# Kernel optimization log

Measured on AMD Instinct MI355X. Metric: run time of the kernel, lower is better.

The kernel has to match this reference:

```python
import jax, jax.numpy as jnp
import numpy as np

N, E, H, IN, ED = 10000, 160000, 8, 128, 32
C1, C2 = 128, 128  # per-head channels of conv1 and conv2_1


def gat_conv(x, edge_index, edge_attr, W, We, att_s, att_d, att_e, bias, concat):
    """PyG GATConv with edge_dim, add_self_loops=True (fill_value='mean'), eval mode."""
    n = x.shape[0]
    h, c = att_s.shape
    src, dst = edge_index[0], edge_index[1]
    # self-loop edge_attr = per-node mean of incoming edge attrs (PyG fill_value='mean')
    deg = jax.ops.segment_sum(jnp.ones((src.shape[0],), x.dtype), dst, num_segments=n)
    loop_attr = jax.ops.segment_sum(edge_attr, dst, num_segments=n) / jnp.maximum(deg, 1.0)[:, None]
    loop = jnp.arange(n)
    src = jnp.concatenate([src, loop])
    dst = jnp.concatenate([dst, loop])
    ea = jnp.concatenate([edge_attr, loop_attr], axis=0)  # [E+N, ED]

    xh = (x @ W).reshape(n, h, c)                  # [N,H,C]
    a_s = jnp.sum(xh * att_s, axis=-1)             # [N,H]
    a_d = jnp.sum(xh * att_d, axis=-1)             # [N,H]
    eh = (ea @ We).reshape(-1, h, c)               # [E+N,H,C]
    a_e = jnp.sum(eh * att_e, axis=-1)             # [E+N,H]

    alpha = jax.nn.leaky_relu(a_s[src] + a_d[dst] + a_e, negative_slope=0.2)
    # segment softmax over incoming edges of each dst node (every node has a self loop)
    amax = jax.ops.segment_max(alpha, dst, num_segments=n)
    ex = jnp.exp(alpha - amax[dst])
    denom = jax.ops.segment_sum(ex, dst, num_segments=n)
    alpha = ex / (denom[dst] + 1e-16)

    out = jax.ops.segment_sum(xh[src] * alpha[:, :, None], dst, num_segments=n)  # [N,H,C]
    out = out.reshape(n, h * c) if concat else out.mean(axis=1)
    return out + bias


def setup_inputs() -> dict:
    key = jax.random.key(0)
    ks = jax.random.split(key, 16)
    s = 0.05
    return {
        "x": jax.random.normal(ks[0], (N, IN), jnp.float32),
        "edge_index": jax.random.randint(ks[1], (2, E), 0, N, dtype=jnp.int64),
        "edge_attr": jax.random.normal(ks[2], (E, ED), jnp.float32),
        # conv1: IN -> H*C1, concat=True
        "W1": jax.random.normal(ks[3], (IN, H * C1), jnp.float32) * s,
        "We1": jax.random.normal(ks[4], (ED, H * C1), jnp.float32) * s,
        "as1": jax.random.normal(ks[5], (H, C1), jnp.float32) * s,
        "ad1": jax.random.normal(ks[6], (H, C1), jnp.float32) * s,
        "ae1": jax.random.normal(ks[7], (H, C1), jnp.float32) * s,
        "b1": jnp.zeros((H * C1,), jnp.float32),
        # conv2_1: H*C1 -> C2, concat=False (Drugbank branch)
        "W2": jax.random.normal(ks[8], (H * C1, H * C2), jnp.float32) * s,
        "We2": jax.random.normal(ks[9], (ED, H * C2), jnp.float32) * s,
        "as2": jax.random.normal(ks[10], (H, C2), jnp.float32) * s,
        "ad2": jax.random.normal(ks[11], (H, C2), jnp.float32) * s,
        "ae2": jax.random.normal(ks[12], (H, C2), jnp.float32) * s,
        "b2": jnp.zeros((C2,), jnp.float32),
    }


def reference(x, edge_index, edge_attr, W1, We1, as1, ad1, ae1, b1,
              W2, We2, as2, ad2, ae2, b2):
    # dataset == 'Drugbank' path; dropout is identity in eval mode
    h = gat_conv(x, edge_index, edge_attr, W1, We1, as1, ad1, ae1, b1, concat=True)
    h = jax.nn.relu(h)
    out = gat_conv(h, edge_index, edge_attr, W2, We2, as2, ad2, ae2, b2, concat=False)
    return out
```

## Files before the change

kernel.cpp:

```cpp
#include <hip/hip_runtime.h>
#include <hip/hip_bf16.h>
#include <cstdint>
#include <cstddef>


#define EDD 32

typedef __attribute__((ext_vector_type(4))) float f32x4;
typedef __attribute__((ext_vector_type(8))) short bf16x8;

__device__ inline unsigned short f2bf_rn(float f) {
  uint32_t u = __float_as_uint(f);
  return (unsigned short)((u + 0x7FFFu + ((u >> 16) & 1u)) >> 16);
}

__device__ inline float bf2f(unsigned short b) {
  return __uint_as_float(((uint32_t)b) << 16);
}

__device__ inline void gload_lds16(const void* g, void* l) {
  __builtin_amdgcn_global_load_lds((const __attribute__((address_space(1))) void*)g,
                                   (__attribute__((address_space(3))) void*)l, 16, 0, 0);
}


__global__ void deg_count_kernel(const int* __restrict__ ei, int* __restrict__ deg, int E) {
  int e = blockIdx.x * 256 + threadIdx.x;
  if (e < E) atomicAdd(&deg[ei[E + e]], 1);
}

__global__ void scan_kernel(const int* __restrict__ deg, int* __restrict__ rowptr,
                            int* __restrict__ cursor, int n) {
  __shared__ int wsum[16];
  int t = threadIdx.x;
  int chunk = (n + 1023) >> 10;
  int lo = min(t * chunk, n), hi = min(lo + chunk, n);
  int s = 0;
  for (int i = lo; i < hi; ++i) s += deg[i];
  int lane = t & 63, w = t >> 6;
  int v = s;
#pragma unroll
  for (int off = 1; off < 64; off <<= 1) {
    int u = __shfl_up(v, off);
    if (lane >= off) v += u;
  }
  if (lane == 63) wsum[w] = v;
  __syncthreads();
  if (t == 0) {
    int acc = 0;
#pragma unroll
    for (int i = 0; i < 16; ++i) { int x = wsum[i]; wsum[i] = acc; acc += x; }
  }
  __syncthreads();
  int excl = v - s + wsum[w];
  for (int i = lo; i < hi; ++i) {
    rowptr[i] = excl; cursor[i] = excl; excl += deg[i];
  }
  if (t == 1023) rowptr[n] = excl;
}

__global__ void scatter_kernel(const int* __restrict__ ei, int* __restrict__ cursor,
                               int* __restrict__ csr_src, int* __restrict__ csr_dst,
                               int* __restrict__ csr_eid, int E) {
  int e = blockIdx.x * 256 + threadIdx.x;
  if (e >= E) return;
  int d = ei[E + e];
  int pos = atomicAdd(&cursor[d], 1);
  csr_src[pos] = ei[e];
  csr_dst[pos] = d;
  csr_eid[pos] = e;
}

__global__ void permute_ea_kernel(const int* __restrict__ csr_eid,
                                  const float* __restrict__ edge_attr,
                                  float* __restrict__ ea_csr, int E) {
  int gid = blockIdx.x * 256 + threadIdx.x;
  if (gid >= E * 8) return;
  int p = gid >> 3, q = gid & 7;
  int e = csr_eid[p];
  ((float4*)ea_csr)[(size_t)p * 8 + q] = ((const float4*)edge_attr)[(size_t)e * 8 + q];
}

__global__ void loop_attr_kernel(const int* __restrict__ rowptr,
                                 const float* __restrict__ ea_csr,
                                 float* __restrict__ loop_attr, int N) {
  int n = blockIdx.x * 8 + (threadIdx.x >> 5);
  int lane = threadIdx.x & 31;
  if (n >= N) return;
  int r0 = rowptr[n], r1 = rowptr[n + 1];
  float s = 0.f;
  for (int p = r0; p < r1; ++p)
    s += ea_csr[(size_t)p * EDD + lane];
  float dv = fmaxf((float)(r1 - r0), 1.f);
  loop_attr[(size_t)n * EDD + lane] = s / dv;
}


__global__ void cvt_bf16_kernel(const float* __restrict__ in,
                                unsigned short* __restrict__ out, int n4) {
  int i = blockIdx.x * 256 + threadIdx.x;
  if (i >= n4) return;
  float4 v = ((const float4*)in)[i];
  ushort4 o;
  o.x = f2bf_rn(v.x); o.y = f2bf_rn(v.y); o.z = f2bf_rn(v.z); o.w = f2bf_rn(v.w);
  ((ushort4*)out)[i] = o;
}

__global__ void transpose_both_kernel(const float* __restrict__ W1, unsigned short* __restrict__ Bt1,
                                      const float* __restrict__ W2, unsigned short* __restrict__ Bt2) {
  __shared__ float tile[32][33];
  int by = blockIdx.y;
  const float* W; unsigned short* Bt; int K, bk;
  if (by < 4) { W = W1; Bt = Bt1; K = 128; bk = by * 32; }
  else        { W = W2; Bt = Bt2; K = 1024; bk = (by - 4) * 32; }
  int bn = blockIdx.x * 32;
  int tx = threadIdx.x & 31, ty = threadIdx.x >> 5;
  for (int r = ty; r < 32; r += 8)
    tile[r][tx] = W[(size_t)(bk + r) * 1024 + bn + tx];
  __syncthreads();
  for (int r = ty; r < 32; r += 8)
    Bt[(size_t)(bn + r) * K + bk + tx] = f2bf_rn(tile[tx][r]);
}

__global__ void ve_both_kernel(const float* __restrict__ We1, const float* __restrict__ ae1,
                               const float* __restrict__ We2, const float* __restrict__ ae2,
                               float* __restrict__ Ve) {
  int b = blockIdx.x;
  const float* We = b ? We2 : We1;
  const float* ae = b ? ae2 : ae1;
  int t = threadIdx.x;
  int d = t >> 3, h = t & 7;
  float s = 0.f;
  for (int c = 0; c < 128; ++c) s = fmaf(We[d * 1024 + h * 128 + c], ae[h * 128 + c], s);
  Ve[b * 256 + t] = s;
}


__global__ __launch_bounds__(256) void gemm1_fullk_kernel(
    const unsigned short* __restrict__ Abf, const unsigned short* __restrict__ Btbf,
    unsigned short* __restrict__ Cbf, float* __restrict__ a_s, float* __restrict__ a_d,
    const float* __restrict__ att_s, const float* __restrict__ att_d, int M) {
  __shared__ __align__(16) unsigned short lds[4 * 8192];
  __shared__ float redS[128][2];
  __shared__ float redD[128][2];
  const int t = threadIdx.x;
  const int lane = t & 63;
  const int wid = t >> 6;
  const int wr = wid >> 1, wc = wid & 1;
  const int m0 = blockIdx.y * 128;
  const int n0 = blockIdx.x * 128;
  const int hb = blockIdx.x;
  const int srow = lane >> 2;
  const int sg = lane & 3;

#pragma unroll
  for (int s = 0; s < 4; ++s) {
    unsigned short* L = lds + s * 8192;
    int k0 = s * 32;
#pragma unroll
    for (int q = 0; q < 2; ++q) {
      int rb = wid * 32 + q * 16;
      int row = rb + srow;
      int gsrc = sg ^ ((row >> 1) & 3);
      size_t ga = (size_t)(m0 + row) * 128 + k0 + gsrc * 8;
      size_t gb = (size_t)(n0 + row) * 128 + k0 + gsrc * 8;
      gload_lds16(Abf + ga, L + rb * 32);
      gload_lds16(Btbf + gb, L + 4096 + rb * 32);
    }
  }
  __syncthreads();

  int offa[4], offb[4];
#pragma unroll
  for (int i = 0; i < 4; ++i) {
    int rowa = wr * 64 + i * 16 + (lane & 15);
    offa[i] = rowa * 32 + (((lane >> 4) ^ ((rowa >> 1) & 3)) * 8);
    int rowb = wc * 64 + i * 16 + (lane & 15);
    offb[i] = rowb * 32 + (((lane >> 4) ^ ((rowb >> 1) & 3)) * 8);
  }

  f32x4 acc[4][4] = {};
#pragma unroll
  for (int s = 0; s < 4; ++s) {
    unsigned short* L = lds + s * 8192;
    bf16x8 ah[4];
#pragma unroll
    for (int i = 0; i < 4; ++i) ah[i] = *(const bf16x8*)(L + offa[i]);
#pragma unroll
    for (int j = 0; j < 4; ++j) {
      bf16x8 bh = *(const bf16x8*)(L + 4096 + offb[j]);
#pragma unroll
      for (int i = 0; i < 4; ++i)
        acc[i][j] = __builtin_amdgcn_mfma_f32_16x16x32_bf16(ah[i], bh, acc[i][j], 0, 0, 0);
    }
  }

  float as_v[4], ad_v[4];
#pragma unroll
  for (int j = 0; j < 4; ++j) {
    int c = n0 + wc * 64 + j * 16 + (lane & 15);
    as_v[j] = att_s[c];
    ad_v[j] = att_d[c];
  }
#pragma unroll
  for (int i = 0; i < 4; ++i) {
#pragma unroll
    for (int r = 0; r < 4; ++r) {
      float sA = 0.f, sD = 0.f;
#pragma unroll
      for (int j = 0; j < 4; ++j) {
        sA = fmaf(acc[i][j][r], as_v[j], sA);
        sD = fmaf(acc[i][j][r], ad_v[j], sD);
      }
#pragma unroll
      for (int mask = 1; mask <= 8; mask <<= 1) {
        sA += __shfl_xor(sA, mask);
        sD += __shfl_xor(sD, mask);
      }
      if ((lane & 15) == 0) {
        int ml = wr * 64 + i * 16 + (lane >> 4) * 4 + r;
        redS[ml][wc] = sA;
        redD[ml][wc] = sD;
      }
      int m = m0 + wr * 64 + i * 16 + (lane >> 4) * 4 + r;
      if (m < M) {
#pragma unroll
        for (int j = 0; j < 4; ++j) {
          int n = n0 + wc * 64 + j * 16 + (lane & 15);
          Cbf[(size_t)m * 1024 + n] = f2bf_rn(acc[i][j][r]);
        }
      }
    }
  }
  __syncthreads();
  if (t < 128) {
    int m = m0 + t;
    if (m < M) {
      a_s[(size_t)m * 8 + hb] = redS[t][0] + redS[t][1];
      a_d[(size_t)m * 8 + hb] = redD[t][0] + redD[t][1];
    }
  }
}


__global__ __launch_bounds__(256) void gemm2_dbuf_kernel(
    const unsigned short* __restrict__ Abf, const unsigned short* __restrict__ Btbf,
    unsigned short* __restrict__ Cbf, float* __restrict__ a_s, float* __restrict__ a_d,
    const float* __restrict__ att_s, const float* __restrict__ att_d, int M, int K) {
  __shared__ __align__(16) unsigned short lds[2 * 8192];
  __shared__ float redS[128][2];
  __shared__ float redD[128][2];
  const int t = threadIdx.x;
  const int lane = t & 63;
  const int wid = t >> 6;
  const int wr = wid >> 1, wc = wid & 1;
  const int m0 = blockIdx.y * 128;
  const int n0 = blockIdx.x * 128;
  const int hb = blockIdx.x;
  const int srow = lane >> 2;
  const int sg = lane & 3;
  const int nk = K >> 5;

  auto stage = [&](int b, int k) {
    unsigned short* L = lds + b * 8192;
    int k0 = k * 32;
#pragma unroll
    for (int q = 0; q < 2; ++q) {
      int rb = wid * 32 + q * 16;
      int row = rb + srow;
      int gsrc = sg ^ ((row >> 1) & 3);
      size_t ga = (size_t)(m0 + row) * K + k0 + gsrc * 8;
      size_t gb = (size_t)(n0 + row) * K + k0 + gsrc * 8;
      gload_lds16(Abf + ga, L + rb * 32);
      gload_lds16(Btbf + gb, L + 4096 + rb * 32);
    }
  };

  int offa[4], offb[4];
#pragma unroll
  for (int i = 0; i < 4; ++i) {
    int rowa = wr * 64 + i * 16 + (lane & 15);
    offa[i] = rowa * 32 + (((lane >> 4) ^ ((rowa >> 1) & 3)) * 8);
    int rowb = wc * 64 + i * 16 + (lane & 15);
    offb[i] = rowb * 32 + (((lane >> 4) ^ ((rowb >> 1) & 3)) * 8);
  }

  f32x4 acc[4][4] = {};
  stage(0, 0);
  __syncthreads();

  for (int k = 0; k < nk; ++k) {
    if (k + 1 < nk) stage((k + 1) & 1, k + 1);
    unsigned short* L = lds + (k & 1) * 8192;
    bf16x8 ah[4], bh[4];
#pragma unroll
    for (int i = 0; i < 4; ++i) ah[i] = *(const bf16x8*)(L + offa[i]);
#pragma unroll
    for (int j = 0; j < 4; ++j) bh[j] = *(const bf16x8*)(L + 4096 + offb[j]);
#pragma unroll
    for (int j = 0; j < 4; ++j)
#pragma unroll
      for (int i = 0; i < 4; ++i)
        acc[i][j] = __builtin_amdgcn_mfma_f32_16x16x32_bf16(ah[i], bh[j], acc[i][j], 0, 0, 0);
    __syncthreads();
  }

  float as_v[4], ad_v[4];
#pragma unroll
  for (int j = 0; j < 4; ++j) {
    int c = n0 + wc * 64 + j * 16 + (lane & 15);
    as_v[j] = att_s[c];
    ad_v[j] = att_d[c];
  }
#pragma unroll
  for (int i = 0; i < 4; ++i) {
#pragma unroll
    for (int r = 0; r < 4; ++r) {
      float sA = 0.f, sD = 0.f;
#pragma unroll
      for (int j = 0; j < 4; ++j) {
        sA = fmaf(acc[i][j][r], as_v[j], sA);
        sD = fmaf(acc[i][j][r], ad_v[j], sD);
      }
#pragma unroll
      for (int mask = 1; mask <= 8; mask <<= 1) {
        sA += __shfl_xor(sA, mask);
        sD += __shfl_xor(sD, mask);
      }
      if ((lane & 15) == 0) {
        int ml = wr * 64 + i * 16 + (lane >> 4) * 4 + r;
        redS[ml][wc] = sA;
        redD[ml][wc] = sD;
      }
      int m = m0 + wr * 64 + i * 16 + (lane >> 4) * 4 + r;
      if (m < M) {
#pragma unroll
        for (int j = 0; j < 4; ++j) {
          int n = n0 + wc * 64 + j * 16 + (lane & 15);
          Cbf[(size_t)m * 1024 + n] = f2bf_rn(acc[i][j][r]);
        }
      }
    }
  }
  __syncthreads();
  if (t < 128) {
    int m = m0 + t;
    if (m < M) {
      a_s[(size_t)m * 8 + hb] = redS[t][0] + redS[t][1];
      a_d[(size_t)m * 8 + hb] = redD[t][0] + redD[t][1];
    }
  }
}


__global__ __launch_bounds__(256) void edge_alpha_kernel(
    const int* __restrict__ csr_src, const int* __restrict__ csr_dst,
    const float* __restrict__ ea_csr, const float* __restrict__ loop_attr,
    const float* __restrict__ a_s, const float* __restrict__ a_d,
    const float* __restrict__ Ve,
    float* __restrict__ alpha_csr, float* __restrict__ alpha_self, int E, int n) {
  __shared__ float sVe[EDD][8];
  int t = threadIdx.x;
  sVe[t >> 3][t & 7] = Ve[t];
  __syncthreads();
  int idx = blockIdx.x * 256 + t;
  if (idx >= E + n) return;
  int s, d;
  const float* ea;
  float* outp;
  if (idx < E) {
    s = csr_src[idx]; d = csr_dst[idx];
    ea = ea_csr + (size_t)idx * EDD;
    outp = alpha_csr + (size_t)idx * 8;
  } else {
    s = d = idx - E;
    ea = loop_attr + (size_t)(idx - E) * EDD;
    outp = alpha_self + (size_t)(idx - E) * 8;
  }
  float ae[8] = {0.f, 0.f, 0.f, 0.f, 0.f, 0.f, 0.f, 0.f};
#pragma unroll
  for (int k = 0; k < EDD; k += 4) {
    float4 v = *(const float4*)&ea[k];
#pragma unroll
    for (int h = 0; h < 8; ++h) {
      ae[h] = fmaf(v.x, sVe[k][h], ae[h]);
      ae[h] = fmaf(v.y, sVe[k + 1][h], ae[h]);
      ae[h] = fmaf(v.z, sVe[k + 2][h], ae[h]);
      ae[h] = fmaf(v.w, sVe[k + 3][h], ae[h]);
    }
  }
#pragma unroll
  for (int h = 0; h < 8; ++h) {
    float a = a_s[(size_t)s * 8 + h] + a_d[(size_t)d * 8 + h] + ae[h];
    outp[h] = (a > 0.f) ? a : 0.2f * a;
  }
}


template <int LAYER>
__global__ __launch_bounds__(256) void agg_fused_kernel(
    const unsigned short* __restrict__ xbf, const float* __restrict__ alpha,
    const float* __restrict__ alpha_self, const int* __restrict__ rowptr,
    const int* __restrict__ csr_src, const float* __restrict__ bias,
    unsigned short* __restrict__ obf, float* __restrict__ outp, int N) {
  int n = blockIdx.x;
  int t = threadIdx.x;
  int lane = t & 63, w = t >> 6;
  __shared__ float wm[4][8], wsm[4][8];
  __shared__ float sm_m[8], sm_inv[8];
  __shared__ int ls[64];
  __shared__ float pws[64 * 8];
  __shared__ float red[256][4];
  int r0 = rowptr[n];
  int deg = rowptr[n + 1] - r0;

  {
    int h = t & 7, slot = t >> 3;
    float m = -1e30f, s = 0.f;
    for (int i = slot; i < deg; i += 32) {
      float a = alpha[(size_t)(r0 + i) * 8 + h];
      if (a <= m) {
        s += __expf(a - m);
      } else {
        s = s * __expf(m - a) + 1.f;
        m = a;
      }
    }
#pragma unroll
    for (int mask = 8; mask < 64; mask <<= 1) {
      float mo = __shfl_xor(m, mask);
      float so = __shfl_xor(s, mask);
      float mn = fmaxf(m, mo);
      s = s * __expf(m - mn) + so * __expf(mo - mn);
      m = mn;
    }
    if (lane < 8) { wm[w][lane] = m; wsm[w][lane] = s; }
  }
  __syncthreads();
  if (t < 8) {
    float m = wm[0][t], s = wsm[0][t];
#pragma unroll
    for (int k = 1; k < 4; ++k) {
      float mo = wm[k][t], so = wsm[k][t];
      float mn = fmaxf(m, mo);
      s = s * __expf(m - mn) + so * __expf(mo - mn);
      m = mn;
    }
    float aself = alpha_self[(size_t)n * 8 + t];
    float mn = fmaxf(m, aself);
    s = s * __expf(m - mn) + __expf(aself - mn);
    sm_m[t] = mn;
    sm_inv[t] = 1.f / (s + 1e-16f);
  }
  __syncthreads();

  int h = t >> 5;
  float m_h = sm_m[h], inv_h = sm_inv[h];
  float m_w = sm_m[t & 7], inv_w = sm_inv[t & 7];
  const ushort4* xv = (const ushort4*)xbf;
  float wself = __expf(alpha_self[(size_t)n * 8 + h] - m_h) * inv_h;
  ushort4 sv = xv[(size_t)n * 256 + t];
  float ax = wself * bf2f(sv.x), ay = wself * bf2f(sv.y);
  float az = wself * bf2f(sv.z), aw = wself * bf2f(sv.w);
  for (int base = 0; base < deg; base += 64) {
    int cnt = min(64, deg - base);
    if (t < cnt) ls[t] = csr_src[r0 + base + t];
    for (int idx = t; idx < cnt * 8; idx += 256)
      pws[idx] = __expf(alpha[(size_t)(r0 + base) * 8 + idx] - m_w) * inv_w;
    __syncthreads();
#pragma unroll 4
    for (int j = 0; j < cnt; ++j) {
      float wt = pws[j * 8 + h];
      ushort4 u = xv[(size_t)ls[j] * 256 + t];
      ax = fmaf(wt, bf2f(u.x), ax);
      ay = fmaf(wt, bf2f(u.y), ay);
      az = fmaf(wt, bf2f(u.z), az);
      aw = fmaf(wt, bf2f(u.w), aw);
    }
    __syncthreads();
  }
  if (LAYER == 1) {
    float4 b = ((const float4*)bias)[t];
    ushort4 o4;
    o4.x = f2bf_rn(fmaxf(ax + b.x, 0.f));
    o4.y = f2bf_rn(fmaxf(ay + b.y, 0.f));
    o4.z = f2bf_rn(fmaxf(az + b.z, 0.f));
    o4.w = f2bf_rn(fmaxf(aw + b.w, 0.f));
    ((ushort4*)obf)[(size_t)n * 256 + t] = o4;
  } else {
    red[t][0] = ax; red[t][1] = ay; red[t][2] = az; red[t][3] = aw;
    __syncthreads();
    if (t < 32) {
      float sx = 0.f, sy = 0.f, sz = 0.f, sw = 0.f;
#pragma unroll
      for (int k = 0; k < 8; ++k) {
        sx += red[t + 32 * k][0];
        sy += red[t + 32 * k][1];
        sz += red[t + 32 * k][2];
        sw += red[t + 32 * k][3];
      }
      float4 b = ((const float4*)bias)[t];
      float4 o;
      o.x = sx * 0.125f + b.x;
      o.y = sy * 0.125f + b.y;
      o.z = sz * 0.125f + b.z;
      o.w = sw * 0.125f + b.w;
      ((float4*)outp)[(size_t)n * 32 + t] = o;
    }
  }
}


extern "C" void kernel_launch(void* const* d_in, const int* in_sizes, int n_in,
                              void* d_out, int out_size, void* d_ws, size_t ws_size,
                              hipStream_t stream) {
  const float* x        = (const float*)d_in[0];
  const int*   ei       = (const int*)d_in[1];
  const float* edge_attr= (const float*)d_in[2];
  const float* W1       = (const float*)d_in[3];
  const float* We1      = (const float*)d_in[4];
  const float* as1      = (const float*)d_in[5];
  const float* ad1      = (const float*)d_in[6];
  const float* ae1      = (const float*)d_in[7];
  const float* b1       = (const float*)d_in[8];
  const float* W2       = (const float*)d_in[9];
  const float* We2      = (const float*)d_in[10];
  const float* as2      = (const float*)d_in[11];
  const float* ad2      = (const float*)d_in[12];
  const float* ae2      = (const float*)d_in[13];
  const float* b2       = (const float*)d_in[14];
  float* out = (float*)d_out;

  const int N = in_sizes[0] / 128;
  const int E = in_sizes[2] / EDD;
  const int Mpad = ((N + 127) / 128) * 128;

  char* ws = (char*)d_ws;
  size_t off = 0;
  auto alloc = [&](size_t bytes) -> void* {
    void* p = ws + off;
    off = (off + bytes + 255) & ~(size_t)255;
    return p;
  };
  int*   deg       = (int*)alloc((size_t)N * 4);
  int*   rowptr    = (int*)alloc((size_t)(N + 1) * 4);
  int*   cursor    = (int*)alloc((size_t)N * 4);
  int*   csr_src   = (int*)alloc((size_t)E * 4);
  int*   csr_dst   = (int*)alloc((size_t)E * 4);
  int*   csr_eid   = (int*)alloc((size_t)E * 4);
  float* ea_csr    = (float*)alloc((size_t)E * EDD * 4);
  float* loop_attr = (float*)alloc((size_t)N * EDD * 4);
  float* a_s       = (float*)alloc((size_t)N * 8 * 4);
  float* a_d       = (float*)alloc((size_t)N * 8 * 4);
  float* Ve        = (float*)alloc(512 * 4);
  float* alpha_csr = (float*)alloc((size_t)E * 8 * 4);
  float* alpha_self= (float*)alloc((size_t)N * 8 * 4);
  unsigned short* xh1bf = (unsigned short*)alloc((size_t)N * 1024 * 2);
  unsigned short* xh2bf = (unsigned short*)alloc((size_t)N * 1024 * 2);
  unsigned short* xbf   = (unsigned short*)alloc((size_t)Mpad * 128 * 2);
  unsigned short* Bt1   = (unsigned short*)alloc((size_t)1024 * 128 * 2);
  unsigned short* Bt2   = (unsigned short*)alloc((size_t)1024 * 1024 * 2);
  unsigned short* h1bf  = (unsigned short*)alloc((size_t)Mpad * 1024 * 2);
  (void)ws_size; (void)n_in; (void)out_size;

  hipMemsetAsync(deg, 0, (size_t)N * 4, stream);

  int gE = (E + 255) / 256;
  deg_count_kernel<<<gE, 256, 0, stream>>>(ei, deg, E);
  scan_kernel<<<1, 1024, 0, stream>>>(deg, rowptr, cursor, N);
  scatter_kernel<<<gE, 256, 0, stream>>>(ei, cursor, csr_src, csr_dst, csr_eid, E);
  permute_ea_kernel<<<(E * 8 + 255) / 256, 256, 0, stream>>>(csr_eid, edge_attr, ea_csr, E);
  loop_attr_kernel<<<(N + 7) / 8, 256, 0, stream>>>(rowptr, ea_csr, loop_attr, N);

  cvt_bf16_kernel<<<(N * 128 / 4 + 255) / 256, 256, 0, stream>>>(x, xbf, N * 128 / 4);
  transpose_both_kernel<<<dim3(32, 36), 256, 0, stream>>>(W1, Bt1, W2, Bt2);
  ve_both_kernel<<<2, 256, 0, stream>>>(We1, ae1, We2, ae2, Ve);

  dim3 ggrid(8, Mpad / 128);
  int gEA = (E + N + 255) / 256;

  gemm1_fullk_kernel<<<ggrid, 256, 0, stream>>>(xbf, Bt1, xh1bf, a_s, a_d, as1, ad1, N);
  edge_alpha_kernel<<<gEA, 256, 0, stream>>>(csr_src, csr_dst, ea_csr, loop_attr,
                                             a_s, a_d, Ve, alpha_csr, alpha_self, E, N);
  agg_fused_kernel<1><<<N, 256, 0, stream>>>(xh1bf, alpha_csr, alpha_self, rowptr, csr_src,
                                             b1, h1bf, nullptr, N);

  gemm2_dbuf_kernel<<<ggrid, 256, 0, stream>>>(h1bf, Bt2, xh2bf, a_s, a_d, as2, ad2, N, 1024);
  edge_alpha_kernel<<<gEA, 256, 0, stream>>>(csr_src, csr_dst, ea_csr, loop_attr,
                                             a_s, a_d, Ve + 256, alpha_csr, alpha_self, E, N);
  agg_fused_kernel<2><<<N, 256, 0, stream>>>(xh2bf, alpha_csr, alpha_self, rowptr, csr_src,
                                             b2, nullptr, out, N);
}
```

Before: 246.3 us.

## Split softmax into separate pass and gather per head with head-major alpha

Alpha is now stored head-major, and a new kernel computes normalized softmax weights in place, one wavefront per node. Aggregation runs one block per (16 nodes, head) so each 16-lane group gathers a 256-byte slice per neighbor, replacing the block-per-node kernel that used shared-memory staging and barriers. Layer 2 writes bf16 per-head partials, and a separate kernel averages the heads and adds the bias. The aim is more parallelism and better L2 locality per head. The cost is extra launches, a bf16 round trip for the layer-2 partial sums, and a strided head-major write pattern in the edge-alpha kernel.

```diff
diff --git a/kernel.cpp b/kernel.cpp
--- a/kernel.cpp
+++ b/kernel.cpp
@@ -8,6 +8,7 @@
 
 typedef __attribute__((ext_vector_type(4))) float f32x4;
 typedef __attribute__((ext_vector_type(8))) short bf16x8;
+typedef __attribute__((ext_vector_type(8))) unsigned short u16x8;
 
 __device__ inline unsigned short f2bf_rn(float f) {
   uint32_t u = __float_as_uint(f);
@@ -353,12 +354,12 @@
 }
 
 
-__global__ __launch_bounds__(256) void edge_alpha_kernel(
+__global__ __launch_bounds__(256) void edge_alpha_t_kernel(
     const int* __restrict__ csr_src, const int* __restrict__ csr_dst,
     const float* __restrict__ ea_csr, const float* __restrict__ loop_attr,
     const float* __restrict__ a_s, const float* __restrict__ a_d,
     const float* __restrict__ Ve,
-    float* __restrict__ alpha_csr, float* __restrict__ alpha_self, int E, int n) {
+    float* __restrict__ alpha_t, float* __restrict__ self_t, int E, int n) {
   __shared__ float sVe[EDD][8];
   int t = threadIdx.x;
   sVe[t >> 3][t & 7] = Ve[t];
@@ -367,15 +368,12 @@
   if (idx >= E + n) return;
   int s, d;
   const float* ea;
-  float* outp;
   if (idx < E) {
     s = csr_src[idx]; d = csr_dst[idx];
     ea = ea_csr + (size_t)idx * EDD;
-    outp = alpha_csr + (size_t)idx * 8;
   } else {
     s = d = idx - E;
     ea = loop_attr + (size_t)(idx - E) * EDD;
-    outp = alpha_self + (size_t)(idx - E) * 8;
   }
   float ae[8] = {0.f, 0.f, 0.f, 0.f, 0.f, 0.f, 0.f, 0.f};
 #pragma unroll
@@ -392,122 +390,124 @@
 #pragma unroll
   for (int h = 0; h < 8; ++h) {
     float a = a_s[(size_t)s * 8 + h] + a_d[(size_t)d * 8 + h] + ae[h];
-    outp[h] = (a > 0.f) ? a : 0.2f * a;
-  }
-}
-
-
-template <int LAYER>
-__global__ __launch_bounds__(256) void agg_fused_kernel(
-    const unsigned short* __restrict__ xbf, const float* __restrict__ alpha,
-    const float* __restrict__ alpha_self, const int* __restrict__ rowptr,
+    a = (a > 0.f) ? a : 0.2f * a;
+    if (idx < E) alpha_t[(size_t)h * E + idx] = a;
+    else         self_t[(size_t)h * n + (idx - E)] = a;
+  }
+}
+
+
+__global__ __launch_bounds__(256) void sm_weights_t_kernel(
+    float* __restrict__ alpha_t, float* __restrict__ self_t,
+    const int* __restrict__ rowptr, int N, int E) {
+  int n = blockIdx.x * 4 + (threadIdx.x >> 6);
+  int lane = threadIdx.x & 63;
+  if (n >= N) return;
+  int r0 = rowptr[n], deg = rowptr[n + 1] - r0;
+  int h = lane >> 3, slot = lane & 7;
+  float* pa = alpha_t + (size_t)h * E + r0;
+  float m = -1e30f, s = 0.f;
+  for (int i = slot; i < deg; i += 8) {
+    float a = pa[i];
+    if (a <= m) {
+      s += __expf(a - m);
+    } else {
+      s = s * __expf(m - a) + 1.f;
+      m = a;
+    }
+  }
+#pragma unroll
+  for (int mask = 1; mask <= 4; mask <<= 1) {
+    float mo = __shfl_xor(m, mask);
+    float so = __shfl_xor(s, mask);
+    float mn = fmaxf(m, mo);
+    s = s * __expf(m - mn) + so * __expf(mo - mn);
+    m = mn;
+  }
+  float aself = self_t[(size_t)h * N + n];
+  float mn = fmaxf(m, aself);
+  s = s * __expf(m - mn) + __expf(aself - mn);
+  float inv = 1.f / (s + 1e-16f);
+  if (slot == 0) self_t[(size_t)h * N + n] = __expf(aself - mn) * inv;
+  for (int i = slot; i < deg; i += 8)
+    pa[i] = __expf(pa[i] - mn) * inv;
+}
+
+
+template <int RELU_BIAS>
+__global__ __launch_bounds__(256) void agg_gather_h_kernel(
+    const unsigned short* __restrict__ xbf, const float* __restrict__ alpha_t,
+    const float* __restrict__ self_t, const int* __restrict__ rowptr,
     const int* __restrict__ csr_src, const float* __restrict__ bias,
-    unsigned short* __restrict__ obf, float* __restrict__ outp, int N) {
-  int n = blockIdx.x;
-  int t = threadIdx.x;
-  int lane = t & 63, w = t >> 6;
-  __shared__ float wm[4][8], wsm[4][8];
-  __shared__ float sm_m[8], sm_inv[8];
-  __shared__ int ls[64];
-  __shared__ float pws[64 * 8];
-  __shared__ float red[256][4];
-  int r0 = rowptr[n];
-  int deg = rowptr[n + 1] - r0;
-
+    unsigned short* __restrict__ obf, int N, int E) {
+  const int h = blockIdx.x & 7;
+  const int g = blockIdx.x >> 3;
+  const int t = threadIdx.x;
+  const int n = g * 16 + (t >> 4);
+  const int sub = t & 15;
+  if (n >= N) return;
+  const int r0 = rowptr[n], r1 = rowptr[n + 1];
+  const float* __restrict__ pw = alpha_t + (size_t)h * E;
+  const size_t cb = (size_t)h * 128 + sub * 8;
+  float acc[8];
   {
-    int h = t & 7, slot = t >> 3;
-    float m = -1e30f, s = 0.f;
-    for (int i = slot; i < deg; i += 32) {
-      float a = alpha[(size_t)(r0 + i) * 8 + h];
-      if (a <= m) {
-        s += __expf(a - m);
-      } else {
-        s = s * __expf(m - a) + 1.f;
-        m = a;
-      }
-    }
-#pragma unroll
-    for (int mask = 8; mask < 64; mask <<= 1) {
-      float mo = __shfl_xor(m, mask);
-      float so = __shfl_xor(s, mask);
-      float mn = fmaxf(m, mo);
-      s = s * __expf(m - mn) + so * __expf(mo - mn);
-      m = mn;
-    }
-    if (lane < 8) { wm[w][lane] = m; wsm[w][lane] = s; }
-  }
-  __syncthreads();
-  if (t < 8) {
-    float m = wm[0][t], s = wsm[0][t];
-#pragma unroll
-    for (int k = 1; k < 4; ++k) {
-      float mo = wm[k][t], so = wsm[k][t];
-      float mn = fmaxf(m, mo);
-      s = s * __expf(m - mn) + so * __expf(mo - mn);
-      m = mn;
-    }
-    float aself = alpha_self[(size_t)n * 8 + t];
-    float mn = fmaxf(m, aself);
-    s = s * __expf(m - mn) + __expf(aself - mn);
-    sm_m[t] = mn;
-    sm_inv[t] = 1.f / (s + 1e-16f);
-  }
-  __syncthreads();
-
-  int h = t >> 5;
-  float m_h = sm_m[h], inv_h = sm_inv[h];
-  float m_w = sm_m[t & 7], inv_w = sm_inv[t & 7];
-  const ushort4* xv = (const ushort4*)xbf;
-  float wself = __expf(alpha_self[(size_t)n * 8 + h] - m_h) * inv_h;
-  ushort4 sv = xv[(size_t)n * 256 + t];
-  float ax = wself * bf2f(sv.x), ay = wself * bf2f(sv.y);
-  float az = wself * bf2f(sv.z), aw = wself * bf2f(sv.w);
-  for (int base = 0; base < deg; base += 64) {
-    int cnt = min(64, deg - base);
-    if (t < cnt) ls[t] = csr_src[r0 + base + t];
-    for (int idx = t; idx < cnt * 8; idx += 256)
-      pws[idx] = __expf(alpha[(size_t)(r0 + base) * 8 + idx] - m_w) * inv_w;
-    __syncthreads();
-#pragma unroll 4
-    for (int j = 0; j < cnt; ++j) {
-      float wt = pws[j * 8 + h];
-      ushort4 u = xv[(size_t)ls[j] * 256 + t];
-      ax = fmaf(wt, bf2f(u.x), ax);
-      ay = fmaf(wt, bf2f(u.y), ay);
-      az = fmaf(wt, bf2f(u.z), az);
-      aw = fmaf(wt, bf2f(u.w), aw);
-    }
-    __syncthreads();
-  }
-  if (LAYER == 1) {
-    float4 b = ((const float4*)bias)[t];
-    ushort4 o4;
-    o4.x = f2bf_rn(fmaxf(ax + b.x, 0.f));
-    o4.y = f2bf_rn(fmaxf(ay + b.y, 0.f));
-    o4.z = f2bf_rn(fmaxf(az + b.z, 0.f));
-    o4.w = f2bf_rn(fmaxf(aw + b.w, 0.f));
-    ((ushort4*)obf)[(size_t)n * 256 + t] = o4;
+    float ws = self_t[(size_t)h * N + n];
+    u16x8 v = *(const u16x8*)(xbf + (size_t)n * 1024 + cb);
+#pragma unroll
+    for (int k = 0; k < 8; ++k) acc[k] = ws * bf2f(v[k]);
+  }
+  int p = r0;
+  for (; p + 2 <= r1; p += 2) {
+    float w0 = pw[p], w1 = pw[p + 1];
+    int s0 = csr_src[p], s1 = csr_src[p + 1];
+    u16x8 v0 = *(const u16x8*)(xbf + (size_t)s0 * 1024 + cb);
+    u16x8 v1 = *(const u16x8*)(xbf + (size_t)s1 * 1024 + cb);
+#pragma unroll
+    for (int k = 0; k < 8; ++k) acc[k] = fmaf(w0, bf2f(v0[k]), acc[k]);
+#pragma unroll
+    for (int k = 0; k < 8; ++k) acc[k] = fmaf(w1, bf2f(v1[k]), acc[k]);
+  }
+  if (p < r1) {
+    float w0 = pw[p];
+    int s0 = csr_src[p];
+    u16x8 v0 = *(const u16x8*)(xbf + (size_t)s0 * 1024 + cb);
+#pragma unroll
+    for (int k = 0; k < 8; ++k) acc[k] = fmaf(w0, bf2f(v0[k]), acc[k]);
+  }
+  u16x8 o;
+  if (RELU_BIAS) {
+    float4 b0 = *(const float4*)(bias + cb);
+    float4 b1v = *(const float4*)(bias + cb + 4);
+    float bb[8] = {b0.x, b0.y, b0.z, b0.w, b1v.x, b1v.y, b1v.z, b1v.w};
+#pragma unroll
+    for (int k = 0; k < 8; ++k) o[k] = f2bf_rn(fmaxf(acc[k] + bb[k], 0.f));
   } else {
-    red[t][0] = ax; red[t][1] = ay; red[t][2] = az; red[t][3] = aw;
-    __syncthreads();
-    if (t < 32) {
-      float sx = 0.f, sy = 0.f, sz = 0.f, sw = 0.f;
-#pragma unroll
-      for (int k = 0; k < 8; ++k) {
-        sx += red[t + 32 * k][0];
-        sy += red[t + 32 * k][1];
-        sz += red[t + 32 * k][2];
-        sw += red[t + 32 * k][3];
-      }
-      float4 b = ((const float4*)bias)[t];
-      float4 o;
-      o.x = sx * 0.125f + b.x;
-      o.y = sy * 0.125f + b.y;
-      o.z = sz * 0.125f + b.z;
-      o.w = sw * 0.125f + b.w;
-      ((float4*)outp)[(size_t)n * 32 + t] = o;
-    }
-  }
+#pragma unroll
+    for (int k = 0; k < 8; ++k) o[k] = f2bf_rn(acc[k]);
+  }
+  *(u16x8*)(obf + (size_t)n * 1024 + cb) = o;
+}
+
+
+__global__ void head_reduce_kernel(const unsigned short* __restrict__ xpart,
+                                   const float* __restrict__ b2,
+                                   float* __restrict__ outp, int N) {
+  int gid = blockIdx.x * 256 + threadIdx.x;
+  if (gid >= N * 32) return;
+  int n = gid >> 5, q = gid & 31;
+  float sx = 0.f, sy = 0.f, sz = 0.f, sw = 0.f;
+#pragma unroll
+  for (int h = 0; h < 8; ++h) {
+    ushort4 v = *(const ushort4*)(xpart + (size_t)n * 1024 + h * 128 + q * 4);
+    sx += bf2f(v.x); sy += bf2f(v.y); sz += bf2f(v.z); sw += bf2f(v.w);
+  }
+  float4 b = ((const float4*)b2)[q];
+  float4 o;
+  o.x = sx * 0.125f + b.x;
+  o.y = sy * 0.125f + b.y;
+  o.z = sz * 0.125f + b.z;
+  o.w = sw * 0.125f + b.w;
+  ((float4*)outp)[(size_t)n * 32 + q] = o;
 }
 
 
@@ -553,10 +553,11 @@
   float* a_s       = (float*)alloc((size_t)N * 8 * 4);
   float* a_d       = (float*)alloc((size_t)N * 8 * 4);
   float* Ve        = (float*)alloc(512 * 4);
-  float* alpha_csr = (float*)alloc((size_t)E * 8 * 4);
-  float* alpha_self= (float*)alloc((size_t)N * 8 * 4);
+  float* alpha_t   = (float*)alloc((size_t)E * 8 * 4);
+  float* self_t    = (float*)alloc((size_t)N * 8 * 4);
   unsigned short* xh1bf = (unsigned short*)alloc((size_t)N * 1024 * 2);
   unsigned short* xh2bf = (unsigned short*)alloc((size_t)N * 1024 * 2);
+  unsigned short* xpart = (unsigned short*)alloc((size_t)N * 1024 * 2);
   unsigned short* xbf   = (unsigned short*)alloc((size_t)Mpad * 128 * 2);
   unsigned short* Bt1   = (unsigned short*)alloc((size_t)1024 * 128 * 2);
   unsigned short* Bt2   = (unsigned short*)alloc((size_t)1024 * 1024 * 2);
@@ -578,16 +579,21 @@
 
   dim3 ggrid(8, Mpad / 128);
   int gEA = (E + N + 255) / 256;
+  int gSM = (N + 3) / 4;
+  int gAG = 8 * ((N + 15) / 16);
 
   gemm1_fullk_kernel<<<ggrid, 256, 0, stream>>>(xbf, Bt1, xh1bf, a_s, a_d, as1, ad1, N);
-  edge_alpha_kernel<<<gEA, 256, 0, stream>>>(csr_src, csr_dst, ea_csr, loop_attr,
-                                             a_s, a_d, Ve, alpha_csr, alpha_self, E, N);
-  agg_fused_kernel<1><<<N, 256, 0, stream>>>(xh1bf, alpha_csr, alpha_self, rowptr, csr_src,
-                                             b1, h1bf, nullptr, N);
+  edge_alpha_t_kernel<<<gEA, 256, 0, stream>>>(csr_src, csr_dst, ea_csr, loop_attr,
+                                               a_s, a_d, Ve, alpha_t, self_t, E, N);
+  sm_weights_t_kernel<<<gSM, 256, 0, stream>>>(alpha_t, self_t, rowptr, N, E);
+  agg_gather_h_kernel<1><<<gAG, 256, 0, stream>>>(xh1bf, alpha_t, self_t, rowptr, csr_src,
+                                                  b1, h1bf, N, E);
 
   gemm2_dbuf_kernel<<<ggrid, 256, 0, stream>>>(h1bf, Bt2, xh2bf, a_s, a_d, as2, ad2, N, 1024);
-  edge_alpha_kernel<<<gEA, 256, 0, stream>>>(csr_src, csr_dst, ea_csr, loop_attr,
-                                             a_s, a_d, Ve + 256, alpha_csr, alpha_self, E, N);
-  agg_fused_kernel<2><<<N, 256, 0, stream>>>(xh2bf, alpha_csr, alpha_self, rowptr, csr_src,
-                                             b2, nullptr, out, N);
-}
+  edge_alpha_t_kernel<<<gEA, 256, 0, stream>>>(csr_src, csr_dst, ea_csr, loop_attr,
+                                               a_s, a_d, Ve + 256, alpha_t, self_t, E, N);
+  sm_weights_t_kernel<<<gSM, 256, 0, stream>>>(alpha_t, self_t, rowptr, N, E);
+  agg_gather_h_kernel<0><<<gAG, 256, 0, stream>>>(xh2bf, alpha_t, self_t, rowptr, csr_src,
+                                                  nullptr, xpart, N, E);
+  head_reduce_kernel<<<(N * 32 + 255) / 256, 256, 0, stream>>>(xpart, b2, out, N);
+}
```

Result: no change. 248.0 us (+0.7%).
